# Kernel tuning notes

Hardware: AMD Instinct MI355X
Metric: run time of the kernel (lower is better)

## Reference

```python
import jax, jax.numpy as jnp
import numpy as np

N = 16384        # total atoms
E = 262144       # edges
D = 128          # dim_embedding
F = 128          # num_filters
G = 50           # num_gaussians
L = 4            # num_interactions
CUTOFF = 5.0
GAMMA = 4.0
NUM_MOLS = 32
LOG2 = float(np.log(2.0))


def ssp(x):
    # ShiftedSoftplus: softplus(x) - log(2)
    return jax.nn.softplus(x) - LOG2


def setup_inputs() -> dict:
    key = jax.random.key(0)
    ks = jax.random.split(key, 24)
    s = lambda *sh: 1.0 / np.sqrt(sh[-2]) if len(sh) >= 2 else 0.1
    inp = {
        "z": jax.random.normal(ks[0], (N, 1), jnp.float32),
        "pos": jax.random.uniform(ks[1], (N, 3), jnp.float32),
        "batch": jnp.sort(jax.random.randint(ks[2], (N,), 0, NUM_MOLS)),
        "edge_src": jax.random.randint(ks[3], (E,), 0, N),
        "edge_dst": jax.random.randint(ks[4], (E,), 0, N),
        # embedding Linear(1, D)
        "emb_W": jax.random.normal(ks[5], (1, D), jnp.float32),
        "emb_b": jax.random.normal(ks[6], (D,), jnp.float32) * 0.1,
        # per-interaction stacked params [L, ...]
        "mlp_W1": jax.random.normal(ks[7], (L, G, F), jnp.float32) / np.sqrt(G),
        "mlp_b1": jnp.zeros((L, F), jnp.float32),
        "mlp_W2": jax.random.normal(ks[8], (L, F, F), jnp.float32) / np.sqrt(F),
        "mlp_b2": jnp.zeros((L, F), jnp.float32),
        "cf1_W": jax.random.normal(ks[9], (L, D, F), jnp.float32) / np.sqrt(D),   # CFConv.lin1 (no bias)
        "cf2_W": jax.random.normal(ks[10], (L, F, D), jnp.float32) / np.sqrt(F),  # CFConv.lin2
        "cf2_b": jnp.zeros((L, D), jnp.float32),
        "int_lin_W": jax.random.normal(ks[11], (L, D, D), jnp.float32) / np.sqrt(D),
        "int_lin_b": jnp.zeros((L, D), jnp.float32),
        # readout head
        "lin1_W": jax.random.normal(ks[12], (D, D // 2), jnp.float32) / np.sqrt(D),
        "lin1_b": jnp.zeros((D // 2,), jnp.float32),
        "lin2_W": jax.random.normal(ks[13], (D // 2, 1), jnp.float32) / np.sqrt(D // 2),
        "lin2_b": jnp.zeros((1,), jnp.float32),
    }
    return inp


def reference(z, pos, batch, edge_src, edge_dst, emb_W, emb_b,
              mlp_W1, mlp_b1, mlp_W2, mlp_b2, cf1_W, cf2_W, cf2_b,
              int_lin_W, int_lin_b, lin1_W, lin1_b, lin2_W, lin2_b):
    # atom embedding: Linear(1, D)
    h = z @ emb_W + emb_b                                  # [N, D]

    # interaction graph distances (graph connectivity precomputed)
    diff = pos[edge_src] - pos[edge_dst]                   # [E, 3]
    dist = jnp.sqrt(jnp.sum(diff * diff, axis=-1) + 1e-12) # [E]

    # radial basis expansion
    mu = jnp.linspace(0.0, CUTOFF, G).astype(h.dtype)      # [G]
    rbf = jnp.exp(-GAMMA * (dist[:, None] - mu) ** 2)      # [E, G]

    # cosine cutoff envelope
    C = 0.5 * (jnp.cos(dist * (np.pi / CUTOFF)) + 1.0)     # [E]

    for l in range(L):
        # continuous filter from RBF: MLP [E,G] -> [E,F]
        Wf = ssp(rbf @ mlp_W1[l] + mlp_b1[l]) @ mlp_W2[l] + mlp_b2[l]
        Wf = Wf * C[:, None]                               # [E, F]
        # CFConv: gather - multiply - scatter-add
        xj = (h @ cf1_W[l])[edge_src]                      # [E, F]
        agg = jax.ops.segment_sum(xj * Wf, edge_dst, num_segments=N)  # [N, F]
        x = agg @ cf2_W[l] + cf2_b[l]                      # [N, D]
        x = ssp(x)
        x = x @ int_lin_W[l] + int_lin_b[l]
        h = h + x                                          # residual

    h = ssp(h @ lin1_W + lin1_b) @ lin2_W + lin2_b         # [N, 1]
    out = jax.ops.segment_sum(h, batch, num_segments=NUM_MOLS)  # [NUM_MOLS, 1]
    return out
```

## Files before the change

kernel.cpp:

```cpp
#include <hip/hip_runtime.h>
#include <hip/hip_bf16.h>
#include <math.h>

#define N_ATOMS 16384
#define N_EDGES 262144
#define DIM 128
#define NF 128
#define NG 50
#define NL 4
#define NMOLS 32
#define EW 8
#define EB 4

typedef short bf16x8 __attribute__((ext_vector_type(8)));
typedef float f32x4 __attribute__((ext_vector_type(4)));

__device__ __forceinline__ float ssp_f(float x) {
    float e = __expf(-fabsf(x));
    return fmaxf(x, 0.0f) + __logf(1.0f + e) - 0.6931471805599453f;
}

__device__ __forceinline__ short f2bf(float x) {
    __hip_bfloat16 b = __float2bfloat16(x);
    return *reinterpret_cast<short*>(&b);
}

__device__ __forceinline__ float bf2f(unsigned short u) {
    unsigned int v = ((unsigned int)u) << 16;
    return __builtin_bit_cast(float, v);
}

__global__ __launch_bounds__(512)
void k_embed_geom(const float* __restrict__ z, const float* __restrict__ Wv,
                  const float* __restrict__ bv, float* __restrict__ h,
                  const float* __restrict__ pos, const int* __restrict__ src,
                  const int* __restrict__ dst, float* __restrict__ dist,
                  float* __restrict__ Cenv) {
    int idx = blockIdx.x * 512 + threadIdx.x;
    int n = idx >> 7, d = idx & 127;
    h[idx] = z[n] * Wv[d] + bv[d];
    if (blockIdx.x < N_EDGES / 512) {
        int e = blockIdx.x * 512 + threadIdx.x;
        int s = src[e], t = dst[e];
        float dx = pos[3*s]   - pos[3*t];
        float dy = pos[3*s+1] - pos[3*t+1];
        float dz = pos[3*s+2] - pos[3*t+2];
        float dd = sqrtf(dx*dx + dy*dy + dz*dz + 1e-12f);
        dist[e] = dd;
        Cenv[e] = 0.5f * (cosf(dd * (float)(M_PI / 5.0)) + 1.0f);
    }
}

__global__ void k_deg(const int* __restrict__ dst, int* __restrict__ deg) {
    int e = blockIdx.x * blockDim.x + threadIdx.x;
    if (e < N_EDGES) atomicAdd(&deg[dst[e]], 1);
}

__global__ __launch_bounds__(1024)
void k_scan(const int* __restrict__ deg, int* __restrict__ cur) {
    __shared__ int tot[1024];
    int t = threadIdx.x;
    int v[16];
    int s = 0;
    #pragma unroll
    for (int j = 0; j < 16; ++j) { int x = deg[t * 16 + j]; v[j] = s; s += x; }
    tot[t] = s;
    __syncthreads();
    for (int off = 1; off < 1024; off <<= 1) {
        int add = (t >= off) ? tot[t - off] : 0;
        __syncthreads();
        tot[t] += add;
        __syncthreads();
    }
    int base = (t == 0) ? 0 : tot[t - 1];
    #pragma unroll
    for (int j = 0; j < 16; ++j) cur[t * 16 + j] = base + v[j];
}

__global__ void k_fill(const int* __restrict__ dst, int* __restrict__ cur,
                       int* __restrict__ edge_of) {
    int e = blockIdx.x * blockDim.x + threadIdx.x;
    if (e < N_EDGES) {
        int p = atomicAdd(&cur[dst[e]], 1);
        edge_of[p] = e;
    }
}

__global__ void k_perm(const int* __restrict__ edge_of, const float* __restrict__ dist,
                       const float* __restrict__ Cenv, const int* __restrict__ src,
                       const int* __restrict__ dst, float* __restrict__ distS,
                       float* __restrict__ CenvS, int* __restrict__ srcS,
                       int* __restrict__ dstS) {
    int p = blockIdx.x * blockDim.x + threadIdx.x;
    if (p >= N_EDGES) return;
    int e = edge_of[p];
    distS[p] = dist[e];
    CenvS[p] = Cenv[e];
    srcS[p]  = src[e];
    dstS[p]  = dst[e];
}

__global__ __launch_bounds__(512)
void k_rbf(const float* __restrict__ distS, short* __restrict__ rbfF) {
    int lane = threadIdx.x & 63;
    int w    = threadIdx.x >> 6;
    int t    = blockIdx.x * 8 + w;
    int q = lane >> 4, m = lane & 15;
    float d = distS[t * 16 + m];
    #pragma unroll
    for (int kc = 0; kc < 2; ++kc) {
        bf16x8 v;
        #pragma unroll
        for (int j = 0; j < 8; ++j) {
            float mu = (float)(kc * 32 + q * 8 + j) * (5.0f / 49.0f);
            float tt = d - mu;
            v[j] = f2bf(__expf(-4.0f * tt * tt));
        }
        *(bf16x8*)&rbfF[(size_t)((t * 2 + kc) * 64 + lane) * 8] = v;
    }
}

__global__ __launch_bounds__(512, 4)
void k_edge_csr(const short* __restrict__ rbfF, const float* __restrict__ CenvS,
                const int* __restrict__ srcS, const int* __restrict__ dstS,
                const float* __restrict__ W1, const float* __restrict__ b1,
                const float* __restrict__ W2, const float* __restrict__ b2,
                const unsigned short* __restrict__ xjb, float* __restrict__ agg)
{
    __shared__ short H1s[64 * 128];
    __shared__ unsigned short msgt[64][136];
    __shared__ int dsts[64];
    __shared__ unsigned long long maskS;
    const int tid  = threadIdx.x;
    const int lane = tid & 63;
    const int w    = tid >> 6;
    const int q    = lane >> 4;
    const int m    = lane & 15;

    bf16x8 W1R[2], W2R[4];
    #pragma unroll
    for (int kc = 0; kc < 2; ++kc) {
        bf16x8 f;
        #pragma unroll
        for (int j = 0; j < 8; ++j) {
            int k = kc * 32 + q * 8 + j;
            float v = (k < NG) ? W1[k * NF + w * 16 + m] : 0.0f;
            f[j] = f2bf(v);
        }
        W1R[kc] = f;
    }
    #pragma unroll
    for (int kc = 0; kc < 4; ++kc) {
        bf16x8 f;
        #pragma unroll
        for (int j = 0; j < 8; ++j) {
            int k = kc * 32 + q * 8 + j;
            f[j] = f2bf(W2[k * NF + w * 16 + m]);
        }
        W2R[kc] = f;
    }
    const float b1v = b1[w * 16 + m];
    const float b2v = b2[w * 16 + m];

    const int nrounds = N_EDGES / 64;
    for (int r = blockIdx.x; r < nrounds; r += gridDim.x) {
        const int p0 = r * 64;
        short* H = H1s;

        #pragma unroll
        for (int a = 0; a < 4; ++a) {
            int tile = r * 4 + a;
            f32x4 acc = {b1v, b1v, b1v, b1v};
            #pragma unroll
            for (int kc = 0; kc < 2; ++kc) {
                bf16x8 A = *(const bf16x8*)&rbfF[(size_t)((tile * 2 + kc) * 64 + lane) * 8];
                acc = __builtin_amdgcn_mfma_f32_16x16x32_bf16(A, W1R[kc], acc, 0, 0, 0);
            }
            #pragma unroll
            for (int i = 0; i < 4; ++i) {
                int e = a * 16 + q * 4 + i;
                int f = w * 16 + m;
                int byte = (e * 256 + f * 2) ^ ((e & 7) << 4);
                *(short*)((char*)H + byte) = f2bf(ssp_f(acc[i]));
            }
        }
        __syncthreads();

        unsigned short xu[4][4];
        #pragma unroll
        for (int a = 0; a < 4; ++a) {
            int4 s4 = *(const int4*)&srcS[p0 + a * 16 + q * 4];
            #pragma unroll
            for (int i = 0; i < 4; ++i)
                xu[a][i] = xjb[(size_t)((const int*)&s4)[i] * NF + w * 16 + m];
        }

        f32x4 acc2[4];
        #pragma unroll
        for (int a = 0; a < 4; ++a) {
            f32x4 acc = {b2v, b2v, b2v, b2v};
            #pragma unroll
            for (int kc = 0; kc < 4; ++kc) {
                int e = a * 16 + m;
                int byte = (e * 256 + (kc * 32 + q * 8) * 2) ^ ((e & 7) << 4);
                bf16x8 A = *(const bf16x8*)((const char*)H + byte);
                acc = __builtin_amdgcn_mfma_f32_16x16x32_bf16(A, W2R[kc], acc, 0, 0, 0);
            }
            acc2[a] = acc;
        }

        #pragma unroll
        for (int a = 0; a < 4; ++a) {
            float4 cc4 = *(const float4*)&CenvS[p0 + a * 16 + q * 4];
            #pragma unroll
            for (int i = 0; i < 4; ++i) {
                float v = acc2[a][i] * ((const float*)&cc4)[i];
                msgt[a * 16 + q * 4 + i][w * 16 + m] =
                    (unsigned short)f2bf(v * bf2f(xu[a][i]));
            }
        }
        if (w == 0) {
            int d = dstS[p0 + lane];
            int prev = __shfl_up(d, 1);
            bool head = (lane == 0) || (d != prev);
            unsigned long long mk = __ballot(head);
            dsts[lane] = d;
            if (lane == 0) maskS = mk;
        }
        __syncthreads();

        {
            int f = tid & 127;
            int g = tid >> 7;
            unsigned long long mm = maskS;
            int k = 0;
            while (mm) {
                int start = __ffsll(mm) - 1;
                mm &= mm - 1;
                int end = mm ? (__ffsll(mm) - 1) : 64;
                if ((k & 3) == g) {
                    float s0 = 0.0f, s1 = 0.0f, s2 = 0.0f, s3 = 0.0f;
                    int p = start;
                    for (; p + 4 <= end; p += 4) {
                        s0 += bf2f(msgt[p    ][f]);
                        s1 += bf2f(msgt[p + 1][f]);
                        s2 += bf2f(msgt[p + 2][f]);
                        s3 += bf2f(msgt[p + 3][f]);
                    }
                    for (; p < end; ++p) s0 += bf2f(msgt[p][f]);
                    float s = (s0 + s1) + (s2 + s3);
                    float* addr = &agg[(size_t)dsts[start] * NF + f];
                    if (start == 0 || end == 64) atomicAdd(addr, s);
                    else *addr = s;
                }
                ++k;
            }
        }
    }
}

template<int ACT, int RESID, int OUTBF>
__global__ __launch_bounds__(512, 2)
void k_node_mfma(const float* __restrict__ in, const float* __restrict__ W,
                 const float* __restrict__ bias, const float* __restrict__ resid,
                 void* __restrict__ outv, float* __restrict__ aggz)
{
    __shared__ short T[32 * 128];
    const int tid  = threadIdx.x;
    const int lane = tid & 63;
    const int w    = tid >> 6;
    const int q    = lane >> 4;
    const int m    = lane & 15;

    bf16x8 WR[4];
    #pragma unroll
    for (int kc = 0; kc < 4; ++kc) {
        bf16x8 f;
        #pragma unroll
        for (int j = 0; j < 8; ++j)
            f[j] = f2bf(W[(kc * 32 + q * 8 + j) * DIM + w * 16 + m]);
        WR[kc] = f;
    }
    const float bv = bias ? bias[w * 16 + m] : 0.0f;

    const int r0 = blockIdx.x * 32;

    {
        int row = tid >> 4;
        int k0  = (tid & 15) * 8;
        const float* src = in + (size_t)(r0 + row) * DIM + k0;
        float4 v0 = *(const float4*)(src);
        float4 v1 = *(const float4*)(src + 4);
        bf16x8 lo;
        #pragma unroll
        for (int j = 0; j < 4; ++j) {
            lo[j]     = f2bf(((const float*)&v0)[j]);
            lo[j + 4] = f2bf(((const float*)&v1)[j]);
        }
        int b0 = (row * 256 + k0 * 2) ^ ((row & 7) << 4);
        *(bf16x8*)((char*)T + b0) = lo;
        if (aggz) {
            float4 zz = {0.0f, 0.0f, 0.0f, 0.0f};
            float* dz = aggz + (size_t)(r0 + row) * DIM + k0;
            *(float4*)dz = zz;
            *(float4*)(dz + 4) = zz;
        }
    }
    __syncthreads();

    #pragma unroll
    for (int a = 0; a < 2; ++a) {
        f32x4 acc = {bv, bv, bv, bv};
        int row = a * 16 + m;
        #pragma unroll
        for (int kc = 0; kc < 4; ++kc) {
            int byte = (row * 256 + (kc * 32 + q * 8) * 2) ^ ((row & 7) << 4);
            bf16x8 A = *(const bf16x8*)((const char*)T + byte);
            acc = __builtin_amdgcn_mfma_f32_16x16x32_bf16(A, WR[kc], acc, 0, 0, 0);
        }
        #pragma unroll
        for (int i = 0; i < 4; ++i) {
            float v = acc[i];
            if (ACT) v = ssp_f(v);
            size_t oi = (size_t)(r0 + a * 16 + q * 4 + i) * DIM + w * 16 + m;
            if (RESID) v += resid[oi];
            if (OUTBF) ((unsigned short*)outv)[oi] = (unsigned short)f2bf(v);
            else       ((float*)outv)[oi] = v;
        }
    }
}

template<int EMIT>
__global__ __launch_bounds__(512, 2)
void k_node_fused(const float* __restrict__ agg, const float* __restrict__ W2,
                  const float* __restrict__ b2, const float* __restrict__ Wi,
                  const float* __restrict__ bi, float* __restrict__ h,
                  const float* __restrict__ W1n, unsigned short* __restrict__ xjn,
                  float* __restrict__ aggz)
{
    __shared__ short T[32 * 128];
    __shared__ short X[32 * 128];
    const int tid  = threadIdx.x;
    const int lane = tid & 63;
    const int w    = tid >> 6;
    const int q    = lane >> 4;
    const int m    = lane & 15;

    bf16x8 W2R[4], WiR[4], W1nR[4];
    #pragma unroll
    for (int kc = 0; kc < 4; ++kc) {
        bf16x8 f2v, fiv;
        #pragma unroll
        for (int j = 0; j < 8; ++j) {
            int k = kc * 32 + q * 8 + j;
            f2v[j] = f2bf(W2[k * DIM + w * 16 + m]);
            fiv[j] = f2bf(Wi[k * DIM + w * 16 + m]);
        }
        W2R[kc] = f2v;
        WiR[kc] = fiv;
    }
    if constexpr (EMIT) {
        #pragma unroll
        for (int kc = 0; kc < 4; ++kc) {
            bf16x8 f;
            #pragma unroll
            for (int j = 0; j < 8; ++j)
                f[j] = f2bf(W1n[(kc * 32 + q * 8 + j) * DIM + w * 16 + m]);
            W1nR[kc] = f;
        }
    }
    const float b2v = b2[w * 16 + m];
    const float biv = bi[w * 16 + m];

    const int r0 = blockIdx.x * 32;
    const int srow = tid >> 4;
    const int sk0  = (tid & 15) * 8;

    {
        const float* src = agg + (size_t)(r0 + srow) * DIM + sk0;
        float4 v0 = *(const float4*)(src);
        float4 v1 = *(const float4*)(src + 4);
        bf16x8 lo;
        #pragma unroll
        for (int j = 0; j < 4; ++j) {
            lo[j]     = f2bf(((const float*)&v0)[j]);
            lo[j + 4] = f2bf(((const float*)&v1)[j]);
        }
        int b0 = (srow * 256 + sk0 * 2) ^ ((srow & 7) << 4);
        *(bf16x8*)((char*)T + b0) = lo;
    }
    __syncthreads();

    #pragma unroll
    for (int a = 0; a < 2; ++a) {
        f32x4 acc = {b2v, b2v, b2v, b2v};
        int row = a * 16 + m;
        #pragma unroll
        for (int kc = 0; kc < 4; ++kc) {
            int byte = (row * 256 + (kc * 32 + q * 8) * 2) ^ ((row & 7) << 4);
            bf16x8 A = *(const bf16x8*)((const char*)T + byte);
            acc = __builtin_amdgcn_mfma_f32_16x16x32_bf16(A, W2R[kc], acc, 0, 0, 0);
        }
        #pragma unroll
        for (int i = 0; i < 4; ++i) {
            int orow = a * 16 + q * 4 + i;
            int ocol = w * 16 + m;
            int byte = (orow * 256 + ocol * 2) ^ ((orow & 7) << 4);
            *(short*)((char*)X + byte) = f2bf(ssp_f(acc[i]));
        }
    }
    __syncthreads();

    #pragma unroll
    for (int a = 0; a < 2; ++a) {
        f32x4 acc = {biv, biv, biv, biv};
        int row = a * 16 + m;
        #pragma unroll
        for (int kc = 0; kc < 4; ++kc) {
            int byte = (row * 256 + (kc * 32 + q * 8) * 2) ^ ((row & 7) << 4);
            bf16x8 A = *(const bf16x8*)((const char*)X + byte);
            acc = __builtin_amdgcn_mfma_f32_16x16x32_bf16(A, WiR[kc], acc, 0, 0, 0);
        }
        #pragma unroll
        for (int i = 0; i < 4; ++i) {
            size_t oi = (size_t)(r0 + a * 16 + q * 4 + i) * DIM + w * 16 + m;
            float v = h[oi] + acc[i];
            h[oi] = v;
            if constexpr (EMIT) {
                int orow = a * 16 + q * 4 + i;
                int ocol = w * 16 + m;
                int byte = (orow * 256 + ocol * 2) ^ ((orow & 7) << 4);
                *(short*)((char*)T + byte) = f2bf(v);
            }
        }
    }

    if constexpr (EMIT) {
        {
            float4 zz = {0.0f, 0.0f, 0.0f, 0.0f};
            float* dz = aggz + (size_t)(r0 + srow) * DIM + sk0;
            *(float4*)dz = zz;
            *(float4*)(dz + 4) = zz;
        }
        __syncthreads();

        #pragma unroll
        for (int a = 0; a < 2; ++a) {
            f32x4 acc = {0.0f, 0.0f, 0.0f, 0.0f};
            int row = a * 16 + m;
            #pragma unroll
            for (int kc = 0; kc < 4; ++kc) {
                int byte = (row * 256 + (kc * 32 + q * 8) * 2) ^ ((row & 7) << 4);
                bf16x8 A = *(const bf16x8*)((const char*)T + byte);
                acc = __builtin_amdgcn_mfma_f32_16x16x32_bf16(A, W1nR[kc], acc, 0, 0, 0);
            }
            #pragma unroll
            for (int i = 0; i < 4; ++i) {
                size_t oi = (size_t)(r0 + a * 16 + q * 4 + i) * DIM + w * 16 + m;
                xjn[oi] = (unsigned short)f2bf(acc[i]);
            }
        }
    }
}

template<int COLS, int ACT, int RESID>
__global__ __launch_bounds__(512)
void k_node_gemm(const float* __restrict__ in, const float* __restrict__ W,
                 const float* __restrict__ bias, const float* __restrict__ resid,
                 float* __restrict__ out)
{
    __shared__ float Ws[DIM][COLS];
    __shared__ float rs[EW][EB][DIM];
    int tid = threadIdx.x;
    for (int i = tid; i < DIM * COLS; i += 512) (&Ws[0][0])[i] = W[i];
    __syncthreads();

    int lane = tid & 63;
    int w = tid >> 6;
    int gw = blockIdx.x * EW + w;
    int nw = gridDim.x * EW;
    int ngroups = N_ATOMS / EB;
    constexpr int CPL = COLS / 64;

    float bb[CPL];
    #pragma unroll
    for (int c = 0; c < CPL; ++c) bb[c] = bias ? bias[lane + 64 * c] : 0.0f;

    for (int grp = gw; grp < ngroups; grp += nw) {
        int r0 = grp * EB;
        #pragma unroll
        for (int r = 0; r < EB; ++r) {
            rs[w][r][lane]      = in[(size_t)(r0 + r) * DIM + lane];
            rs[w][r][lane + 64] = in[(size_t)(r0 + r) * DIM + lane + 64];
        }
        float acc[EB][CPL];
        #pragma unroll
        for (int r = 0; r < EB; ++r)
            #pragma unroll
            for (int c = 0; c < CPL; ++c) acc[r][c] = bb[c];
        #pragma unroll 2
        for (int kb = 0; kb < DIM / 4; ++kb) {
            float4 rv[EB];
            #pragma unroll
            for (int r = 0; r < EB; ++r)
                rv[r] = *(const float4*)&rs[w][r][4 * kb];
            #pragma unroll
            for (int j = 0; j < 4; ++j) {
                float wv[CPL];
                #pragma unroll
                for (int c = 0; c < CPL; ++c) wv[c] = Ws[4 * kb + j][lane + 64 * c];
                #pragma unroll
                for (int r = 0; r < EB; ++r) {
                    float rj = ((const float*)&rv[r])[j];
                    #pragma unroll
                    for (int c = 0; c < CPL; ++c)
                        acc[r][c] = fmaf(rj, wv[c], acc[r][c]);
                }
            }
        }
        #pragma unroll
        for (int r = 0; r < EB; ++r) {
            #pragma unroll
            for (int c = 0; c < CPL; ++c) {
                float v = acc[r][c];
                if (ACT) v = ssp_f(v);
                size_t oi = (size_t)(r0 + r) * COLS + lane + 64 * c;
                if (RESID) v += resid[oi];
                out[oi] = v;
            }
        }
    }
}

__global__ __launch_bounds__(256)
void k_final(const float* __restrict__ r1, const float* __restrict__ l2W,
             const float* __restrict__ l2b, const int* __restrict__ batch,
             float* __restrict__ out)
{
    __shared__ float mols[NMOLS];
    int tid = threadIdx.x;
    if (tid < NMOLS) mols[tid] = 0.0f;
    __syncthreads();

    int n = blockIdx.x * 256 + tid;
    const float4* row = (const float4*)(r1 + (size_t)n * 64);
    const float4* wv  = (const float4*)l2W;
    float s = 0.0f;
    #pragma unroll
    for (int k = 0; k < 16; ++k) {
        float4 a = row[k], b = wv[k];
        s += a.x * b.x + a.y * b.y + a.z * b.z + a.w * b.w;
    }
    s += l2b[0];
    atomicAdd(&mols[batch[n]], s);
    __syncthreads();
    if (tid < NMOLS) atomicAdd(&out[tid], mols[tid]);
}

extern "C" void kernel_launch(void* const* d_in, const int* in_sizes, int n_in,
                              void* d_out, int out_size, void* d_ws, size_t ws_size,
                              hipStream_t stream) {
    const float* z     = (const float*)d_in[0];
    const float* pos   = (const float*)d_in[1];
    const int*   batch = (const int*)d_in[2];
    const int*   esrc  = (const int*)d_in[3];
    const int*   edst  = (const int*)d_in[4];
    const float* embW  = (const float*)d_in[5];
    const float* embB  = (const float*)d_in[6];
    const float* mlpW1 = (const float*)d_in[7];
    const float* mlpB1 = (const float*)d_in[8];
    const float* mlpW2 = (const float*)d_in[9];
    const float* mlpB2 = (const float*)d_in[10];
    const float* cf1W  = (const float*)d_in[11];
    const float* cf2W  = (const float*)d_in[12];
    const float* cf2B  = (const float*)d_in[13];
    const float* intW  = (const float*)d_in[14];
    const float* intB  = (const float*)d_in[15];
    const float* l1W   = (const float*)d_in[16];
    const float* l1B   = (const float*)d_in[17];
    const float* l2W   = (const float*)d_in[18];
    const float* l2B   = (const float*)d_in[19];
    float* out = (float*)d_out;

    char* ws = (char*)d_ws;
    float* h     = (float*)(ws);
    float* dist  = (float*)(ws + (size_t)( 8 << 20));
    float* Cv    = (float*)(ws + (size_t)( 9 << 20));
    unsigned short* xj = (unsigned short*)(ws + (size_t)(10 << 20));
    float* agg   = (float*)(ws + (size_t)(18 << 20));
    short* rbfF  = (short*)(ws + (size_t)(26 << 20));
    int*   deg   = (int*)  (ws + (size_t)(58 << 20));
    int*   cur   = (int*)  (ws + (size_t)(59 << 20));
    int*   edge_of = (int*)(ws + (size_t)(60 << 20));
    float* distS = (float*)(ws + (size_t)(61 << 20));
    float* CenvS = (float*)(ws + (size_t)(62 << 20));
    int*   srcS  = (int*)  (ws + (size_t)(63 << 20));
    int*   dstS  = (int*)  (ws + (size_t)(64 << 20));
    float* r1    = agg;

    k_embed_geom<<<dim3(N_ATOMS * DIM / 512), dim3(512), 0, stream>>>(
        z, embW, embB, h, pos, esrc, edst, dist, Cv);

    hipMemsetAsync(deg, 0, N_ATOMS * sizeof(int), stream);
    k_deg<<<dim3(N_EDGES / 512), dim3(512), 0, stream>>>(edst, deg);
    k_scan<<<dim3(1), dim3(1024), 0, stream>>>(deg, cur);
    k_fill<<<dim3(N_EDGES / 512), dim3(512), 0, stream>>>(edst, cur, edge_of);
    k_perm<<<dim3(N_EDGES / 512), dim3(512), 0, stream>>>(edge_of, dist, Cv, esrc, edst,
                                                          distS, CenvS, srcS, dstS);
    k_rbf<<<dim3(N_EDGES / 16 / 8), dim3(512), 0, stream>>>(distS, rbfF);

    k_node_mfma<0, 0, 1><<<dim3(N_ATOMS / 32), dim3(512), 0, stream>>>(
        h, cf1W, nullptr, nullptr, (void*)xj, agg);

    for (int l = 0; l < NL; ++l) {
        k_edge_csr<<<dim3(1024), dim3(512), 0, stream>>>(
            rbfF, CenvS, srcS, dstS,
            mlpW1 + (size_t)l * NG * NF, mlpB1 + (size_t)l * NF,
            mlpW2 + (size_t)l * NF * NF, mlpB2 + (size_t)l * NF,
            xj, agg);
        if (l < NL - 1) {
            k_node_fused<1><<<dim3(N_ATOMS / 32), dim3(512), 0, stream>>>(
                agg, cf2W + (size_t)l * NF * DIM, cf2B + (size_t)l * DIM,
                intW + (size_t)l * DIM * DIM, intB + (size_t)l * DIM, h,
                cf1W + (size_t)(l + 1) * DIM * NF, xj, agg);
        } else {
            k_node_fused<0><<<dim3(N_ATOMS / 32), dim3(512), 0, stream>>>(
                agg, cf2W + (size_t)l * NF * DIM, cf2B + (size_t)l * DIM,
                intW + (size_t)l * DIM * DIM, intB + (size_t)l * DIM, h,
                nullptr, nullptr, nullptr);
        }
    }

    k_node_gemm<64, 1, 0><<<dim3(256), dim3(512), 0, stream>>>(h, l1W, l1B, nullptr, r1);
    hipMemsetAsync(out, 0, NMOLS * sizeof(float), stream);
    k_final<<<dim3(N_ATOMS / 256), dim3(256), 0, stream>>>(r1, l2W, l2B, batch, out);
}
```

Before: 463.6 us.

## Fuse degree count, RBF expansion and readout head into neighbouring kernels

```diff
diff --git a/kernel.cpp b/kernel.cpp
--- a/kernel.cpp
+++ b/kernel.cpp
@@ -10,7 +10,6 @@
 #define NL 4
 #define NMOLS 32
 #define EW 8
-#define EB 4
 
 typedef short bf16x8 __attribute__((ext_vector_type(8)));
 typedef float f32x4 __attribute__((ext_vector_type(4)));
@@ -35,7 +34,7 @@
                   const float* __restrict__ bv, float* __restrict__ h,
                   const float* __restrict__ pos, const int* __restrict__ src,
                   const int* __restrict__ dst, float* __restrict__ dist,
-                  float* __restrict__ Cenv) {
+                  float* __restrict__ Cenv, int* __restrict__ deg) {
     int idx = blockIdx.x * 512 + threadIdx.x;
     int n = idx >> 7, d = idx & 127;
     h[idx] = z[n] * Wv[d] + bv[d];
@@ -48,12 +47,8 @@
         float dd = sqrtf(dx*dx + dy*dy + dz*dz + 1e-12f);
         dist[e] = dd;
         Cenv[e] = 0.5f * (cosf(dd * (float)(M_PI / 5.0)) + 1.0f);
-    }
-}
-
-__global__ void k_deg(const int* __restrict__ dst, int* __restrict__ deg) {
-    int e = blockIdx.x * blockDim.x + threadIdx.x;
-    if (e < N_EDGES) atomicAdd(&deg[dst[e]], 1);
+        atomicAdd(&deg[t], 1);
+    }
 }
 
 __global__ __launch_bounds__(1024)
@@ -86,37 +81,33 @@
     }
 }
 
-__global__ void k_perm(const int* __restrict__ edge_of, const float* __restrict__ dist,
-                       const float* __restrict__ Cenv, const int* __restrict__ src,
-                       const int* __restrict__ dst, float* __restrict__ distS,
-                       float* __restrict__ CenvS, int* __restrict__ srcS,
-                       int* __restrict__ dstS) {
+__global__ __launch_bounds__(512)
+void k_perm_rbf(const int* __restrict__ edge_of, const float* __restrict__ dist,
+                const float* __restrict__ Cenv, const int* __restrict__ src,
+                const int* __restrict__ dst, float* __restrict__ CenvS,
+                int* __restrict__ srcS, int* __restrict__ dstS,
+                short* __restrict__ rbfF) {
     int p = blockIdx.x * blockDim.x + threadIdx.x;
     if (p >= N_EDGES) return;
     int e = edge_of[p];
-    distS[p] = dist[e];
+    float d = dist[e];
     CenvS[p] = Cenv[e];
     srcS[p]  = src[e];
     dstS[p]  = dst[e];
-}
-
-__global__ __launch_bounds__(512)
-void k_rbf(const float* __restrict__ distS, short* __restrict__ rbfF) {
-    int lane = threadIdx.x & 63;
-    int w    = threadIdx.x >> 6;
-    int t    = blockIdx.x * 8 + w;
-    int q = lane >> 4, m = lane & 15;
-    float d = distS[t * 16 + m];
+    int t = p >> 4, m = p & 15;
     #pragma unroll
     for (int kc = 0; kc < 2; ++kc) {
-        bf16x8 v;
-        #pragma unroll
-        for (int j = 0; j < 8; ++j) {
-            float mu = (float)(kc * 32 + q * 8 + j) * (5.0f / 49.0f);
-            float tt = d - mu;
-            v[j] = f2bf(__expf(-4.0f * tt * tt));
-        }
-        *(bf16x8*)&rbfF[(size_t)((t * 2 + kc) * 64 + lane) * 8] = v;
+        #pragma unroll
+        for (int q = 0; q < 4; ++q) {
+            bf16x8 v;
+            #pragma unroll
+            for (int j = 0; j < 8; ++j) {
+                float mu = (float)(kc * 32 + q * 8 + j) * (5.0f / 49.0f);
+                float tt = d - mu;
+                v[j] = f2bf(__expf(-4.0f * tt * tt));
+            }
+            *(bf16x8*)&rbfF[(size_t)((t * 2 + kc) * 64 + q * 16 + m) * 8] = v;
+        }
     }
 }
 
@@ -330,23 +321,30 @@
     }
 }
 
-template<int EMIT>
+template<int EMIT, int FINAL>
 __global__ __launch_bounds__(512, 2)
 void k_node_fused(const float* __restrict__ agg, const float* __restrict__ W2,
                   const float* __restrict__ b2, const float* __restrict__ Wi,
                   const float* __restrict__ bi, float* __restrict__ h,
                   const float* __restrict__ W1n, unsigned short* __restrict__ xjn,
-                  float* __restrict__ aggz)
+                  float* __restrict__ aggz,
+                  const float* __restrict__ l1W, const float* __restrict__ l1B,
+                  const float* __restrict__ l2W, const float* __restrict__ l2b,
+                  const int* __restrict__ batch, float* __restrict__ out)
 {
     __shared__ short T[32 * 128];
     __shared__ short X[32 * 128];
+    __shared__ float part[32][4];
+    __shared__ float molsS[NMOLS];
     const int tid  = threadIdx.x;
     const int lane = tid & 63;
     const int w    = tid >> 6;
     const int q    = lane >> 4;
     const int m    = lane & 15;
 
-    bf16x8 W2R[4], WiR[4], W1nR[4];
+    if (FINAL && tid < NMOLS) molsS[tid] = 0.0f;
+
+    bf16x8 W2R[4], WiR[4], W1nR[4], L1R[4];
     #pragma unroll
     for (int kc = 0; kc < 4; ++kc) {
         bf16x8 f2v, fiv;
@@ -367,6 +365,18 @@
             for (int j = 0; j < 8; ++j)
                 f[j] = f2bf(W1n[(kc * 32 + q * 8 + j) * DIM + w * 16 + m]);
             W1nR[kc] = f;
+        }
+    }
+    if constexpr (FINAL) {
+        if (w < 4) {
+            #pragma unroll
+            for (int kc = 0; kc < 4; ++kc) {
+                bf16x8 f;
+                #pragma unroll
+                for (int j = 0; j < 8; ++j)
+                    f[j] = f2bf(l1W[(kc * 32 + q * 8 + j) * 64 + w * 16 + m]);
+                L1R[kc] = f;
+            }
         }
     }
     const float b2v = b2[w * 16 + m];
@@ -426,7 +436,7 @@
             size_t oi = (size_t)(r0 + a * 16 + q * 4 + i) * DIM + w * 16 + m;
             float v = h[oi] + acc[i];
             h[oi] = v;
-            if constexpr (EMIT) {
+            if constexpr (EMIT || FINAL) {
                 int orow = a * 16 + q * 4 + i;
                 int ocol = w * 16 + m;
                 int byte = (orow * 256 + ocol * 2) ^ ((orow & 7) << 4);
@@ -436,14 +446,14 @@
     }
 
     if constexpr (EMIT) {
-        {
-            float4 zz = {0.0f, 0.0f, 0.0f, 0.0f};
-            float* dz = aggz + (size_t)(r0 + srow) * DIM + sk0;
-            *(float4*)dz = zz;
-            *(float4*)(dz + 4) = zz;
-        }
-        __syncthreads();
-
+        float4 zz = {0.0f, 0.0f, 0.0f, 0.0f};
+        float* dz = aggz + (size_t)(r0 + srow) * DIM + sk0;
+        *(float4*)dz = zz;
+        *(float4*)(dz + 4) = zz;
+    }
+    if constexpr (EMIT || FINAL) __syncthreads();
+
+    if constexpr (EMIT) {
         #pragma unroll
         for (int a = 0; a < 2; ++a) {
             f32x4 acc = {0.0f, 0.0f, 0.0f, 0.0f};
@@ -461,100 +471,41 @@
             }
         }
     }
-}
-
-template<int COLS, int ACT, int RESID>
-__global__ __launch_bounds__(512)
-void k_node_gemm(const float* __restrict__ in, const float* __restrict__ W,
-                 const float* __restrict__ bias, const float* __restrict__ resid,
-                 float* __restrict__ out)
-{
-    __shared__ float Ws[DIM][COLS];
-    __shared__ float rs[EW][EB][DIM];
-    int tid = threadIdx.x;
-    for (int i = tid; i < DIM * COLS; i += 512) (&Ws[0][0])[i] = W[i];
-    __syncthreads();
-
-    int lane = tid & 63;
-    int w = tid >> 6;
-    int gw = blockIdx.x * EW + w;
-    int nw = gridDim.x * EW;
-    int ngroups = N_ATOMS / EB;
-    constexpr int CPL = COLS / 64;
-
-    float bb[CPL];
-    #pragma unroll
-    for (int c = 0; c < CPL; ++c) bb[c] = bias ? bias[lane + 64 * c] : 0.0f;
-
-    for (int grp = gw; grp < ngroups; grp += nw) {
-        int r0 = grp * EB;
-        #pragma unroll
-        for (int r = 0; r < EB; ++r) {
-            rs[w][r][lane]      = in[(size_t)(r0 + r) * DIM + lane];
-            rs[w][r][lane + 64] = in[(size_t)(r0 + r) * DIM + lane + 64];
-        }
-        float acc[EB][CPL];
-        #pragma unroll
-        for (int r = 0; r < EB; ++r)
-            #pragma unroll
-            for (int c = 0; c < CPL; ++c) acc[r][c] = bb[c];
-        #pragma unroll 2
-        for (int kb = 0; kb < DIM / 4; ++kb) {
-            float4 rv[EB];
-            #pragma unroll
-            for (int r = 0; r < EB; ++r)
-                rv[r] = *(const float4*)&rs[w][r][4 * kb];
-            #pragma unroll
-            for (int j = 0; j < 4; ++j) {
-                float wv[CPL];
+
+    if constexpr (FINAL) {
+        if (w < 4) {
+            const float l1bv = l1B[w * 16 + m];
+            const float l2wv = l2W[w * 16 + m];
+            #pragma unroll
+            for (int a = 0; a < 2; ++a) {
+                f32x4 acc = {l1bv, l1bv, l1bv, l1bv};
+                int row = a * 16 + m;
                 #pragma unroll
-                for (int c = 0; c < CPL; ++c) wv[c] = Ws[4 * kb + j][lane + 64 * c];
+                for (int kc = 0; kc < 4; ++kc) {
+                    int byte = (row * 256 + (kc * 32 + q * 8) * 2) ^ ((row & 7) << 4);
+                    bf16x8 A = *(const bf16x8*)((const char*)T + byte);
+                    acc = __builtin_amdgcn_mfma_f32_16x16x32_bf16(A, L1R[kc], acc, 0, 0, 0);
+                }
                 #pragma unroll
-                for (int r = 0; r < EB; ++r) {
-                    float rj = ((const float*)&rv[r])[j];
+                for (int i = 0; i < 4; ++i) {
+                    float v = ssp_f(acc[i]) * l2wv;
                     #pragma unroll
-                    for (int c = 0; c < CPL; ++c)
-                        acc[r][c] = fmaf(rj, wv[c], acc[r][c]);
+                    for (int off = 1; off < 16; off <<= 1) v += __shfl_xor(v, off);
+                    if (m == 0) part[a * 16 + q * 4 + i][w] = v;
                 }
             }
         }
-        #pragma unroll
-        for (int r = 0; r < EB; ++r) {
-            #pragma unroll
-            for (int c = 0; c < CPL; ++c) {
-                float v = acc[r][c];
-                if (ACT) v = ssp_f(v);
-                size_t oi = (size_t)(r0 + r) * COLS + lane + 64 * c;
-                if (RESID) v += resid[oi];
-                out[oi] = v;
-            }
-        }
-    }
-}
-
-__global__ __launch_bounds__(256)
-void k_final(const float* __restrict__ r1, const float* __restrict__ l2W,
-             const float* __restrict__ l2b, const int* __restrict__ batch,
-             float* __restrict__ out)
-{
-    __shared__ float mols[NMOLS];
-    int tid = threadIdx.x;
-    if (tid < NMOLS) mols[tid] = 0.0f;
-    __syncthreads();
-
-    int n = blockIdx.x * 256 + tid;
-    const float4* row = (const float4*)(r1 + (size_t)n * 64);
-    const float4* wv  = (const float4*)l2W;
-    float s = 0.0f;
-    #pragma unroll
-    for (int k = 0; k < 16; ++k) {
-        float4 a = row[k], b = wv[k];
-        s += a.x * b.x + a.y * b.y + a.z * b.z + a.w * b.w;
-    }
-    s += l2b[0];
-    atomicAdd(&mols[batch[n]], s);
-    __syncthreads();
-    if (tid < NMOLS) atomicAdd(&out[tid], mols[tid]);
+        __syncthreads();
+        if (tid < 32) {
+            float s = part[tid][0] + part[tid][1] + part[tid][2] + part[tid][3] + l2b[0];
+            atomicAdd(&molsS[batch[r0 + tid]], s);
+        }
+        __syncthreads();
+        if (tid < NMOLS) {
+            float v = molsS[tid];
+            if (v != 0.0f) atomicAdd(&out[tid], v);
+        }
+    }
 }
 
 extern "C" void kernel_launch(void* const* d_in, const int* in_sizes, int n_in,
@@ -592,22 +543,19 @@
     int*   deg   = (int*)  (ws + (size_t)(58 << 20));
     int*   cur   = (int*)  (ws + (size_t)(59 << 20));
     int*   edge_of = (int*)(ws + (size_t)(60 << 20));
-    float* distS = (float*)(ws + (size_t)(61 << 20));
     float* CenvS = (float*)(ws + (size_t)(62 << 20));
     int*   srcS  = (int*)  (ws + (size_t)(63 << 20));
     int*   dstS  = (int*)  (ws + (size_t)(64 << 20));
-    float* r1    = agg;
+
+    hipMemsetAsync(deg, 0, N_ATOMS * sizeof(int), stream);
+    hipMemsetAsync(out, 0, NMOLS * sizeof(float), stream);
 
     k_embed_geom<<<dim3(N_ATOMS * DIM / 512), dim3(512), 0, stream>>>(
-        z, embW, embB, h, pos, esrc, edst, dist, Cv);
-
-    hipMemsetAsync(deg, 0, N_ATOMS * sizeof(int), stream);
-    k_deg<<<dim3(N_EDGES / 512), dim3(512), 0, stream>>>(edst, deg);
+        z, embW, embB, h, pos, esrc, edst, dist, Cv, deg);
     k_scan<<<dim3(1), dim3(1024), 0, stream>>>(deg, cur);
     k_fill<<<dim3(N_EDGES / 512), dim3(512), 0, stream>>>(edst, cur, edge_of);
-    k_perm<<<dim3(N_EDGES / 512), dim3(512), 0, stream>>>(edge_of, dist, Cv, esrc, edst,
-                                                          distS, CenvS, srcS, dstS);
-    k_rbf<<<dim3(N_EDGES / 16 / 8), dim3(512), 0, stream>>>(distS, rbfF);
+    k_perm_rbf<<<dim3(N_EDGES / 512), dim3(512), 0, stream>>>(
+        edge_of, dist, Cv, esrc, edst, CenvS, srcS, dstS, rbfF);
 
     k_node_mfma<0, 0, 1><<<dim3(N_ATOMS / 32), dim3(512), 0, stream>>>(
         h, cf1W, nullptr, nullptr, (void*)xj, agg);
@@ -619,19 +567,17 @@
             mlpW2 + (size_t)l * NF * NF, mlpB2 + (size_t)l * NF,
             xj, agg);
         if (l < NL - 1) {
-            k_node_fused<1><<<dim3(N_ATOMS / 32), dim3(512), 0, stream>>>(
+            k_node_fused<1, 0><<<dim3(N_ATOMS / 32), dim3(512), 0, stream>>>(
                 agg, cf2W + (size_t)l * NF * DIM, cf2B + (size_t)l * DIM,
                 intW + (size_t)l * DIM * DIM, intB + (size_t)l * DIM, h,
-                cf1W + (size_t)(l + 1) * DIM * NF, xj, agg);
+                cf1W + (size_t)(l + 1) * DIM * NF, xj, agg,
+                nullptr, nullptr, nullptr, nullptr, nullptr, nullptr);
         } else {
-            k_node_fused<0><<<dim3(N_ATOMS / 32), dim3(512), 0, stream>>>(
+            k_node_fused<0, 1><<<dim3(N_ATOMS / 32), dim3(512), 0, stream>>>(
                 agg, cf2W + (size_t)l * NF * DIM, cf2B + (size_t)l * DIM,
                 intW + (size_t)l * DIM * DIM, intB + (size_t)l * DIM, h,
-                nullptr, nullptr, nullptr);
-        }
-    }
-
-    k_node_gemm<64, 1, 0><<<dim3(256), dim3(512), 0, stream>>>(h, l1W, l1B, nullptr, r1);
-    hipMemsetAsync(out, 0, NMOLS * sizeof(float), stream);
-    k_final<<<dim3(N_ATOMS / 256), dim3(256), 0, stream>>>(r1, l2W, l2B, batch, out);
-}
+                nullptr, nullptr, nullptr,
+                l1W, l1B, l2W, l2B, batch, out);
+        }
+    }
+}
```

Measured after the change: 449.2 us, median of 2. 1.03x faster.
